# Kernel optimization log

Hardware: AMD Instinct MI355X
Metric: run time of the kernel (lower is better)

## Reference

```python
import jax, jax.numpy as jnp
import numpy as np

N_NODES, N_EDGES = 4096, 8192
NODE_FEAT, EDGE_FEAT = 64, 32
NODE_EMB, EDGE_EMB = 64, 64
SPARSITY = 0.002  # ~ avg degree 16 for edge-to-edge graph


def setup_inputs() -> dict:
    key = jax.random.key(0)
    ks = jax.random.split(key, 8)
    node_features = jax.random.normal(ks[0], (N_NODES, NODE_FEAT), jnp.float32)
    edge_features = jax.random.normal(ks[1], (N_EDGES, EDGE_FEAT), jnp.float32)
    # binary adjacency matrices (graph structure), stored dense float as in the original
    edge_to_edge = (jax.random.uniform(ks[2], (N_EDGES, N_EDGES)) < SPARSITY).astype(jnp.float32)
    node_to_edge = (jax.random.uniform(ks[3], (N_NODES, N_EDGES)) < SPARSITY).astype(jnp.float32)
    # xavier-uniform params
    def xavier(k, shape):
        lim = np.sqrt(6.0 / (shape[0] + shape[-1]))
        return jax.random.uniform(k, shape, jnp.float32, -lim, lim)
    W_node = xavier(ks[4], (NODE_FEAT, NODE_EMB))
    W_edge = xavier(ks[5], (EDGE_FEAT, EDGE_EMB))
    p_edge = jax.random.normal(ks[6], (2 * EDGE_EMB,), jnp.float32)
    p_node = jax.random.normal(ks[7], (EDGE_EMB + NODE_EMB,), jnp.float32)
    return {
        "node_features": node_features,
        "edge_features": edge_features,
        "edge_to_edge_adj_matrix": edge_to_edge,
        "node_to_edge_adj_matrix": node_to_edge,
        "W_node": W_node,
        "W_edge": W_edge,
        "p_edge": p_edge,
        "p_node": p_node,
    }


def reference(node_features, edge_features, edge_to_edge_adj_matrix,
              node_to_edge_adj_matrix, W_node, W_edge, p_edge, p_node):
    lrelu = jax.nn.leaky_relu  # default slope 0.01 == torch LeakyReLU
    n_nodes = node_features.shape[0]
    n_edges = edge_features.shape[0]
    d_e = W_edge.shape[1]

    node_embeds = node_features @ W_node          # [N, d_n]
    edge_embeds = edge_features @ W_edge          # [E, d_e]
    A_n = node_to_edge_adj_matrix.T               # [E, N]
    A_e = edge_to_edge_adj_matrix.T               # [E, E]

    # --- node-level attention ---
    # original: cat(repeat(edge_embeds), diag_embed(A_n) @ node_embeds) . p_node
    # == edge_embeds@p1 (broadcast over n) + A_n * (node_embeds@p2)
    s_self_n = edge_embeds @ p_node[:d_e]         # [E]
    s_nb_n = node_embeds @ p_node[d_e:]           # [N]
    att_n = lrelu(s_self_n[:, None] + A_n * s_nb_n[None, :])   # [E, N]
    coef_n = jax.nn.softmax(att_n, axis=1)
    # mean_n over n of coef*A_n[e,n]*node_features[n]
    means_n = (coef_n * A_n) @ node_features / n_nodes          # [E, node_feat]
    out_nodes = lrelu(means_n @ W_node)                         # [E, d_n]

    # --- edge-level attention ---
    s_self_e = edge_embeds @ p_edge[:d_e]         # [E]
    s_nb_e = edge_embeds @ p_edge[d_e:]           # [E]
    att_e = lrelu(s_self_e[:, None] + A_e * s_nb_e[None, :])    # [E, E]
    coef_e = jax.nn.softmax(att_e, axis=1)
    means_e = (coef_e * A_e) @ edge_features / n_edges          # [E, edge_feat]
    out_edges = lrelu(means_e @ W_edge)                         # [E, d_e]

    return jnp.concatenate([out_nodes, out_edges], axis=1)      # [E, d_n + d_e]
```

## Files before the change

kernel.cpp:

```cpp
#include <hip/hip_runtime.h>

constexpr int E = 8192;
constexpr int N = 4096;
constexpr int CAP = 64;

typedef float f4 __attribute__((ext_vector_type(4)));

__device__ __forceinline__ float lrelu(float x) { return x > 0.f ? x : 0.01f * x; }

__device__ __forceinline__ float wave_sum(float v) {
  #pragma unroll
  for (int m = 1; m < 64; m <<= 1) v += __shfl_xor(v, m, 64);
  return v;
}

__global__ __launch_bounds__(256) void scores_k(
    const float* __restrict__ ef, const float* __restrict__ We,
    const float* __restrict__ nf, const float* __restrict__ Wn,
    const float* __restrict__ pe, const float* __restrict__ pn,
    float* __restrict__ s_self_e, float* __restrict__ s_nb_e,
    float* __restrict__ s_self_n, float* __restrict__ s_nb_n,
    int* __restrict__ cnt_base)
{
  const int gtid = blockIdx.x * 256 + threadIdx.x;
  if (gtid < 2 * E) cnt_base[gtid] = 0;

  const int wave = threadIdx.x >> 6, lane = threadIdx.x & 63;
  if (blockIdx.x < E / 4) {
    const int j = blockIdx.x * 4 + wave;
    float emb = 0.f;
    #pragma unroll
    for (int k = 0; k < 32; ++k) emb = fmaf(ef[j * 32 + k], We[k * 64 + lane], emb);
    float a = wave_sum(emb * pe[lane]);
    float b = wave_sum(emb * pe[64 + lane]);
    float c = wave_sum(emb * pn[lane]);
    if (lane == 0) { s_self_e[j] = a; s_nb_e[j] = b; s_self_n[j] = c; }
  } else {
    const int n = (blockIdx.x - E / 4) * 4 + wave;
    float emb = 0.f;
    #pragma unroll
    for (int k = 0; k < 64; ++k) emb = fmaf(nf[n * 64 + k], Wn[k * 64 + lane], emb);
    float b = wave_sum(emb * pn[64 + lane]);
    if (lane == 0) s_nb_n[n] = b;
  }
}

__global__ __launch_bounds__(256) void build_k(
    const f4* __restrict__ e2e, const f4* __restrict__ n2e,
    int* __restrict__ cnt_e, int* __restrict__ idx_e,
    int* __restrict__ cnt_n, int* __restrict__ idx_n)
{
  constexpr int n4_e = E * E / 4;
  constexpr int n4_n = N * E / 4;
  const int stride = gridDim.x * blockDim.x;
  for (int i = blockIdx.x * blockDim.x + threadIdx.x; i < n4_e + n4_n; i += stride) {
    const bool is_e = i < n4_e;
    const f4* __restrict__ src = is_e ? e2e : (n2e - n4_e);
    const f4 v = __builtin_nontemporal_load(&src[i]);
    if (v.x != 0.f || v.y != 0.f || v.z != 0.f || v.w != 0.f) {
      int* cnt = is_e ? cnt_e : cnt_n;
      int* idx = is_e ? idx_e : idx_n;
      const int flat = (is_e ? i : i - n4_e) << 2;
      const int c = flat & (E - 1);
      const int r = flat >> 13;
      if (v.x != 0.f) { int s = atomicAdd(&cnt[c    ], 1); if (s < CAP) idx[(c    ) * CAP + s] = r; }
      if (v.y != 0.f) { int s = atomicAdd(&cnt[c + 1], 1); if (s < CAP) idx[(c + 1) * CAP + s] = r; }
      if (v.z != 0.f) { int s = atomicAdd(&cnt[c + 2], 1); if (s < CAP) idx[(c + 2) * CAP + s] = r; }
      if (v.w != 0.f) { int s = atomicAdd(&cnt[c + 3], 1); if (s < CAP) idx[(c + 3) * CAP + s] = r; }
    }
  }
}

__global__ __launch_bounds__(128) void phase_b_k(
    const int* __restrict__ cnt_e, const int* __restrict__ idx_e,
    const int* __restrict__ cnt_n, const int* __restrict__ idx_n,
    const float* __restrict__ s_self_e, const float* __restrict__ s_nb_e,
    const float* __restrict__ s_self_n, const float* __restrict__ s_nb_n,
    const float* __restrict__ edge_features, const float* __restrict__ node_features,
    const float* __restrict__ W_edge, const float* __restrict__ W_node,
    float* __restrict__ out)
{
  __shared__ float w_sh[2][64];
  __shared__ int   j_sh[2][64];
  __shared__ float mean_sh[2][64];

  const int e    = blockIdx.x;
  const int wave = threadIdx.x >> 6;
  const int lane = threadIdx.x & 63;

  const int   cnt     = wave ? cnt_e[e] : cnt_n[e];
  const int   deg     = min(cnt, CAP);
  const int*  idx     = wave ? (idx_e + e * CAP) : (idx_n + e * CAP);
  const float s_self  = wave ? s_self_e[e] : s_self_n[e];
  const float* s_nb   = wave ? s_nb_e : s_nb_n;
  const float* feat   = wave ? edge_features : node_features;
  const int   fdim    = wave ? 32 : 64;
  const int   total   = wave ? E : N;
  const float inv_cnt = wave ? (1.f / E) : (1.f / N);
  const float* W      = wave ? W_edge : W_node;

  int j = 0;
  if (lane < deg) j = idx[lane];
  j_sh[wave][lane] = j;
  __syncthreads();
  int rank = 0;
  if (lane < deg)
    for (int t = 0; t < deg; ++t) rank += (j_sh[wave][t] < j);
  __syncthreads();
  if (lane < deg) j_sh[wave][rank] = j;
  __syncthreads();
  j = j_sh[wave][lane];

  const float shift = lrelu(s_self);
  float w = 0.f;
  if (lane < deg) w = expf(lrelu(s_self + s_nb[j]) - shift);
  w_sh[wave][lane] = w;
  const float denom = (float)(total - cnt) + wave_sum(w);
  __syncthreads();

  float m = 0.f;
  if (lane < fdim) {
    for (int t = 0; t < deg; ++t)
      m = fmaf(w_sh[wave][t], feat[j_sh[wave][t] * fdim + lane], m);
    m = m / denom * inv_cnt;
  }
  mean_sh[wave][lane] = m;
  __syncthreads();

  float acc = 0.f;
  for (int f = 0; f < fdim; ++f)
    acc = fmaf(mean_sh[wave][f], W[f * 64 + lane], acc);
  out[e * 128 + wave * 64 + lane] = lrelu(acc);
}

extern "C" void kernel_launch(void* const* d_in, const int* in_sizes, int n_in,
                              void* d_out, int out_size, void* d_ws, size_t ws_size,
                              hipStream_t stream)
{
  const float* node_features = (const float*)d_in[0];
  const float* edge_features = (const float*)d_in[1];
  const float* e2e           = (const float*)d_in[2];
  const float* n2e           = (const float*)d_in[3];
  const float* W_node        = (const float*)d_in[4];
  const float* W_edge        = (const float*)d_in[5];
  const float* p_edge        = (const float*)d_in[6];
  const float* p_node        = (const float*)d_in[7];
  float* out = (float*)d_out;

  char* ws = (char*)d_ws;
  int*   cnt_e    = (int*)ws;   ws += (size_t)E * 4;
  int*   cnt_n    = (int*)ws;   ws += (size_t)E * 4;
  int*   idx_e    = (int*)ws;   ws += (size_t)E * CAP * 4;
  int*   idx_n    = (int*)ws;   ws += (size_t)E * CAP * 4;
  float* s_self_e = (float*)ws; ws += (size_t)E * 4;
  float* s_nb_e   = (float*)ws; ws += (size_t)E * 4;
  float* s_self_n = (float*)ws; ws += (size_t)E * 4;
  float* s_nb_n   = (float*)ws; ws += (size_t)N * 4;

  scores_k<<<E / 4 + N / 4, 256, 0, stream>>>(
      edge_features, W_edge, node_features, W_node, p_edge, p_node,
      s_self_e, s_nb_e, s_self_n, s_nb_n, cnt_e );

  build_k<<<2048, 256, 0, stream>>>((const f4*)e2e, (const f4*)n2e,
                                    cnt_e, idx_e, cnt_n, idx_n);

  phase_b_k<<<E, 128, 0, stream>>>(cnt_e, idx_e, cnt_n, idx_n,
                                   s_self_e, s_nb_e, s_self_n, s_nb_n,
                                   edge_features, node_features,
                                   W_edge, W_node, out);
}
```

Baseline: 105.3 us.

## Split adjacency scan by matrix and make phase_b wave-independent without block syncs

```diff
diff --git a/kernel.cpp b/kernel.cpp
--- a/kernel.cpp
+++ b/kernel.cpp
@@ -45,6 +45,19 @@
   }
 }
 
+__device__ __forceinline__ void proc_f4(const f4 v, int flat,
+                                        int* __restrict__ cnt, int* __restrict__ idx)
+{
+  if (v.x != 0.f || v.y != 0.f || v.z != 0.f || v.w != 0.f) {
+    const int c = flat & (E - 1);
+    const int r = flat >> 13;
+    if (v.x != 0.f) { int s = atomicAdd(&cnt[c    ], 1); if (s < CAP) idx[(c    ) * CAP + s] = r; }
+    if (v.y != 0.f) { int s = atomicAdd(&cnt[c + 1], 1); if (s < CAP) idx[(c + 1) * CAP + s] = r; }
+    if (v.z != 0.f) { int s = atomicAdd(&cnt[c + 2], 1); if (s < CAP) idx[(c + 2) * CAP + s] = r; }
+    if (v.w != 0.f) { int s = atomicAdd(&cnt[c + 3], 1); if (s < CAP) idx[(c + 3) * CAP + s] = r; }
+  }
+}
+
 __global__ __launch_bounds__(256) void build_k(
     const f4* __restrict__ e2e, const f4* __restrict__ n2e,
     int* __restrict__ cnt_e, int* __restrict__ idx_e,
@@ -52,26 +65,24 @@
 {
   constexpr int n4_e = E * E / 4;
   constexpr int n4_n = N * E / 4;
-  const int stride = gridDim.x * blockDim.x;
-  for (int i = blockIdx.x * blockDim.x + threadIdx.x; i < n4_e + n4_n; i += stride) {
-    const bool is_e = i < n4_e;
-    const f4* __restrict__ src = is_e ? e2e : (n2e - n4_e);
-    const f4 v = __builtin_nontemporal_load(&src[i]);
-    if (v.x != 0.f || v.y != 0.f || v.z != 0.f || v.w != 0.f) {
-      int* cnt = is_e ? cnt_e : cnt_n;
-      int* idx = is_e ? idx_e : idx_n;
-      const int flat = (is_e ? i : i - n4_e) << 2;
-      const int c = flat & (E - 1);
-      const int r = flat >> 13;
-      if (v.x != 0.f) { int s = atomicAdd(&cnt[c    ], 1); if (s < CAP) idx[(c    ) * CAP + s] = r; }
-      if (v.y != 0.f) { int s = atomicAdd(&cnt[c + 1], 1); if (s < CAP) idx[(c + 1) * CAP + s] = r; }
-      if (v.z != 0.f) { int s = atomicAdd(&cnt[c + 2], 1); if (s < CAP) idx[(c + 2) * CAP + s] = r; }
-      if (v.w != 0.f) { int s = atomicAdd(&cnt[c + 3], 1); if (s < CAP) idx[(c + 3) * CAP + s] = r; }
+  constexpr int BLK_E = 1366;
+
+  if (blockIdx.x < BLK_E) {
+    const int stride = BLK_E * 256;
+    for (int i = (int)blockIdx.x * 256 + (int)threadIdx.x; i < n4_e; i += stride) {
+      const f4 v = __builtin_nontemporal_load(&e2e[i]);
+      proc_f4(v, i << 2, cnt_e, idx_e);
+    }
+  } else {
+    const int stride = (2048 - BLK_E) * 256;
+    for (int i = ((int)blockIdx.x - BLK_E) * 256 + (int)threadIdx.x; i < n4_n; i += stride) {
+      const f4 v = n2e[i];
+      proc_f4(v, i << 2, cnt_n, idx_n);
     }
   }
 }
 
-__global__ __launch_bounds__(128) void phase_b_k(
+__global__ __launch_bounds__(512) void phase_b_k(
     const int* __restrict__ cnt_e, const int* __restrict__ idx_e,
     const int* __restrict__ cnt_n, const int* __restrict__ idx_n,
     const float* __restrict__ s_self_e, const float* __restrict__ s_nb_e,
@@ -80,57 +91,55 @@
     const float* __restrict__ W_edge, const float* __restrict__ W_node,
     float* __restrict__ out)
 {
-  __shared__ float w_sh[2][64];
-  __shared__ int   j_sh[2][64];
-  __shared__ float mean_sh[2][64];
+  __shared__ float w_sh[8][64];
+  __shared__ int   j_sh[8][64];
+  __shared__ int   js_sh[8][64];
+  __shared__ float mean_sh[8][64];
 
-  const int e    = blockIdx.x;
-  const int wave = threadIdx.x >> 6;
+  const int w    = threadIdx.x >> 6;
   const int lane = threadIdx.x & 63;
+  const int gw   = blockIdx.x * 8 + w;
+  const int e    = gw >> 1;
+  const int lvl  = gw & 1;
 
-  const int   cnt     = wave ? cnt_e[e] : cnt_n[e];
+  const int   cnt     = lvl ? cnt_e[e] : cnt_n[e];
   const int   deg     = min(cnt, CAP);
-  const int*  idx     = wave ? (idx_e + e * CAP) : (idx_n + e * CAP);
-  const float s_self  = wave ? s_self_e[e] : s_self_n[e];
-  const float* s_nb   = wave ? s_nb_e : s_nb_n;
-  const float* feat   = wave ? edge_features : node_features;
-  const int   fdim    = wave ? 32 : 64;
-  const int   total   = wave ? E : N;
-  const float inv_cnt = wave ? (1.f / E) : (1.f / N);
-  const float* W      = wave ? W_edge : W_node;
+  const int*  idx     = lvl ? (idx_e + e * CAP) : (idx_n + e * CAP);
+  const float s_self  = lvl ? s_self_e[e] : s_self_n[e];
+  const float* s_nb   = lvl ? s_nb_e : s_nb_n;
+  const float* feat   = lvl ? edge_features : node_features;
+  const int   fdim    = lvl ? 32 : 64;
+  const int   total   = lvl ? E : N;
+  const float inv_cnt = lvl ? (1.f / E) : (1.f / N);
+  const float* W      = lvl ? W_edge : W_node;
 
   int j = 0;
   if (lane < deg) j = idx[lane];
-  j_sh[wave][lane] = j;
-  __syncthreads();
+  j_sh[w][lane] = j;
   int rank = 0;
   if (lane < deg)
-    for (int t = 0; t < deg; ++t) rank += (j_sh[wave][t] < j);
-  __syncthreads();
-  if (lane < deg) j_sh[wave][rank] = j;
-  __syncthreads();
-  j = j_sh[wave][lane];
+    for (int t = 0; t < deg; ++t) rank += (j_sh[w][t] < j);
+  if (lane < deg) js_sh[w][rank] = j;
+  j = js_sh[w][lane];
 
   const float shift = lrelu(s_self);
-  float w = 0.f;
-  if (lane < deg) w = expf(lrelu(s_self + s_nb[j]) - shift);
-  w_sh[wave][lane] = w;
-  const float denom = (float)(total - cnt) + wave_sum(w);
-  __syncthreads();
+  float wgt = 0.f;
+  if (lane < deg) wgt = expf(lrelu(s_self + s_nb[j]) - shift);
+  w_sh[w][lane] = wgt;
+  const float denom = (float)(total - cnt) + wave_sum(wgt);
 
   float m = 0.f;
   if (lane < fdim) {
     for (int t = 0; t < deg; ++t)
-      m = fmaf(w_sh[wave][t], feat[j_sh[wave][t] * fdim + lane], m);
+      m = fmaf(w_sh[w][t], feat[js_sh[w][t] * fdim + lane], m);
     m = m / denom * inv_cnt;
   }
-  mean_sh[wave][lane] = m;
-  __syncthreads();
+  mean_sh[w][lane] = m;
 
   float acc = 0.f;
   for (int f = 0; f < fdim; ++f)
-    acc = fmaf(mean_sh[wave][f], W[f * 64 + lane], acc);
-  out[e * 128 + wave * 64 + lane] = lrelu(acc);
+    acc = fmaf(mean_sh[w][f], W[f * 64 + lane], acc);
+  out[e * 128 + lvl * 64 + lane] = lrelu(acc);
 }
 
 extern "C" void kernel_launch(void* const* d_in, const int* in_sizes, int n_in,
@@ -164,8 +173,8 @@
   build_k<<<2048, 256, 0, stream>>>((const f4*)e2e, (const f4*)n2e,
                                     cnt_e, idx_e, cnt_n, idx_n);
 
-  phase_b_k<<<E, 128, 0, stream>>>(cnt_e, idx_e, cnt_n, idx_n,
-                                   s_self_e, s_nb_e, s_self_n, s_nb_n,
-                                   edge_features, node_features,
-                                   W_edge, W_node, out);
+  phase_b_k<<<E * 2 / 8, 512, 0, stream>>>(cnt_e, idx_e, cnt_n, idx_n,
+                                           s_self_e, s_nb_e, s_self_n, s_nb_n,
+                                           edge_features, node_features,
+                                           W_edge, W_node, out);
 }
```

Result: faster. 96.87 us (-8.0%).
